# Optimization experiments

Measured on AMD Instinct MI355X. Metric: run time of the kernel, lower is better.

The kernel has to match this reference:

```python
import jax, jax.numpy as jnp
import numpy as np

N = 1_000_000
NUM_CLASSES = 100
N_BINS = 15


def setup_inputs() -> dict:
    key = jax.random.key(0)
    k1, k2 = jax.random.split(key)
    logits = jax.random.normal(k1, (N, NUM_CLASSES), dtype=jnp.float32)
    labels = jax.random.randint(k2, (N,), 0, NUM_CLASSES, dtype=jnp.int64)
    return {"logits": logits, "labels": labels, "n_bins": N_BINS}


def reference(logits, labels, n_bins):
    # softmax -> per-sample confidence (max prob) and prediction (argmax)
    softmaxes = jax.nn.softmax(logits, axis=1)
    confidences = jnp.max(softmaxes, axis=1)
    predictions = jnp.argmax(softmaxes, axis=1).astype(jnp.int32)
    accuracies = (predictions == labels.astype(jnp.int32)).astype(confidences.dtype)

    num_classes = logits.shape[1]
    num_data = logits.shape[0]

    # Bin assignment matching (lower, upper] intervals of linspace(0,1,n_bins+1):
    # conf in ((b)/n_bins, (b+1)/n_bins] -> bin b. conf > 0 always (softmax max).
    bin_idx = jnp.clip(
        jnp.ceil(confidences * n_bins).astype(jnp.int32) - 1, 0, n_bins - 1
    )
    # Fused cell id over (predicted class, bin)
    cell = predictions * n_bins + bin_idx  # [N]
    num_cells = num_classes * n_bins

    sum_conf = jax.ops.segment_sum(confidences, cell, num_segments=num_cells)
    sum_acc = jax.ops.segment_sum(accuracies, cell, num_segments=num_cells)

    # Per non-empty cell: |mean_conf - mean_acc| * count/N = |sum_conf - sum_acc|/N;
    # empty cells contribute exactly 0.
    ece = jnp.sum(jnp.abs(sum_conf - sum_acc)) / num_data
    return ece
```

## Files before the change

### kernel.cpp

```cpp
#include <hip/hip_runtime.h>
#include <math.h>


constexpr int C  = 100;
constexpr int NB = 15;
constexpr int NCELLS = C * NB;

__global__ void ece_zero(float* __restrict__ ws, int n) {
    int i = blockIdx.x * blockDim.x + threadIdx.x;
    if (i < n) ws[i] = 0.0f;
}

__global__ __launch_bounds__(256)
void ece_main(const float* __restrict__ logits,
              const int* __restrict__ labels,
              int N, float* __restrict__ cellsums) {
    __shared__ float hist[2 * NCELLS];
    for (int i = threadIdx.x; i < 2 * NCELLS; i += blockDim.x) hist[i] = 0.0f;
    __syncthreads();

    const int lane4   = threadIdx.x & 3;
    const int group   = (blockIdx.x * blockDim.x + threadIdx.x) >> 2;
    const int ngroups = (gridDim.x * blockDim.x) >> 2;

    for (int row = group; row < N; row += ngroups) {
        const float4* p = reinterpret_cast<const float4*>(logits + (size_t)row * C);

        float4 v[6];
        #pragma unroll
        for (int j = 0; j < 6; ++j) v[j] = p[lane4 + 4 * j];
        const bool has7 = (lane4 == 0);
        float4 v6;
        if (has7) v6 = p[24];

        float m = -INFINITY;
        int   am = 0;
        #pragma unroll
        for (int j = 0; j < 6; ++j) {
            int base = (lane4 + 4 * j) * 4;
            if (v[j].x > m) { m = v[j].x; am = base + 0; }
            if (v[j].y > m) { m = v[j].y; am = base + 1; }
            if (v[j].z > m) { m = v[j].z; am = base + 2; }
            if (v[j].w > m) { m = v[j].w; am = base + 3; }
        }
        if (has7) {
            if (v6.x > m) { m = v6.x; am = 96; }
            if (v6.y > m) { m = v6.y; am = 97; }
            if (v6.z > m) { m = v6.z; am = 98; }
            if (v6.w > m) { m = v6.w; am = 99; }
        }

        #pragma unroll
        for (int off = 1; off < 4; off <<= 1) {
            float om  = __shfl_xor(m, off, 64);
            int   oam = __shfl_xor(am, off, 64);
            if (om > m || (om == m && oam < am)) { m = om; am = oam; }
        }

        float s = 0.0f;
        #pragma unroll
        for (int j = 0; j < 6; ++j) {
            s += __expf(v[j].x - m) + __expf(v[j].y - m)
               + __expf(v[j].z - m) + __expf(v[j].w - m);
        }
        if (has7) {
            s += __expf(v6.x - m) + __expf(v6.y - m)
               + __expf(v6.z - m) + __expf(v6.w - m);
        }
        #pragma unroll
        for (int off = 1; off < 4; off <<= 1) s += __shfl_xor(s, off, 64);

        if (lane4 == 0) {
            float conf = 1.0f / s;
            int b = (int)ceilf(conf * (float)NB) - 1;
            b = b < 0 ? 0 : (b > NB - 1 ? NB - 1 : b);
            int cell = am * NB + b;
            atomicAdd(&hist[cell], conf);
            if (labels[row] == am) atomicAdd(&hist[NCELLS + cell], 1.0f);
        }
    }

    __syncthreads();
    for (int i = threadIdx.x; i < 2 * NCELLS; i += blockDim.x) {
        float v = hist[i];
        if (v != 0.0f) atomicAdd(&cellsums[i], v);
    }
}

__global__ void ece_final(const float* __restrict__ cellsums,
                          float invN, float* __restrict__ out) {
    __shared__ float red[256];
    float t = 0.0f;
    for (int i = threadIdx.x; i < NCELLS; i += blockDim.x)
        t += fabsf(cellsums[i] - cellsums[NCELLS + i]);
    red[threadIdx.x] = t;
    __syncthreads();
    for (int w = 128; w > 0; w >>= 1) {
        if (threadIdx.x < w) red[threadIdx.x] += red[threadIdx.x + w];
        __syncthreads();
    }
    if (threadIdx.x == 0) out[0] = red[0] * invN;
}

extern "C" void kernel_launch(void* const* d_in, const int* in_sizes, int n_in,
                              void* d_out, int out_size, void* d_ws, size_t ws_size,
                              hipStream_t stream) {
    const float* logits = (const float*)d_in[0];
    const int*   labels = (const int*)d_in[1];

    const int N = in_sizes[1];

    float* cellsums = (float*)d_ws;
    float* out = (float*)d_out;

    {
        int n = 2 * NCELLS;
        ece_zero<<<(n + 255) / 256, 256, 0, stream>>>(cellsums, n);
    }

    ece_main<<<2048, 256, 0, stream>>>(logits, labels, N, cellsums);

    ece_final<<<1, 256, 0, stream>>>(cellsums, 1.0f / (float)N, out);
}
```

Measured before the change: 103.6 us.

## Stage logits tiles into LDS via global_load_lds before per-row softmax

The main kernel now copies tiles of 64 rows into padded LDS with the direct global-to-LDS load builtin, using fully contiguous 16-byte lane accesses. Each 4-lane group then reads its row from LDS instead of issuing strided global loads. The grid shrinks to 977 blocks, and exp is rewritten as exp2f of an FMA with log2(e). The aim is better-coalesced, higher-throughput HBM reads. In exchange, each tile costs two block barriers with no double buffering, and the added LDS use per block lowers occupancy.

```diff
diff --git a/kernel.cpp b/kernel.cpp
--- a/kernel.cpp
+++ b/kernel.cpp
@@ -5,82 +5,122 @@
 constexpr int C  = 100;
 constexpr int NB = 15;
 constexpr int NCELLS = C * NB;
+constexpr int ROWS_PER_TILE = 64;
+constexpr int F4_PER_ROW   = 25;
+constexpr int LDS_F4_STRIDE = 26;
+constexpr int LDS_TILE_F4  = ROWS_PER_TILE * LDS_F4_STRIDE;
+constexpr int GRID_MAIN = 977;
 
 __global__ void ece_zero(float* __restrict__ ws, int n) {
     int i = blockIdx.x * blockDim.x + threadIdx.x;
     if (i < n) ws[i] = 0.0f;
 }
 
+__device__ __forceinline__ void load_lds_16B(const void* gsrc, void* ldst) {
+    __builtin_amdgcn_global_load_lds(
+        (const __attribute__((address_space(1))) void*)gsrc,
+        (__attribute__((address_space(3))) void*)ldst, 16, 0, 0);
+}
+
 __global__ __launch_bounds__(256)
 void ece_main(const float* __restrict__ logits,
               const int* __restrict__ labels,
-              int N, float* __restrict__ cellsums) {
-    __shared__ float hist[2 * NCELLS];
+              int N, int ntiles, float* __restrict__ cellsums) {
+    __shared__ float4 stage[LDS_TILE_F4];
+    __shared__ float  hist[2 * NCELLS];
+
     for (int i = threadIdx.x; i < 2 * NCELLS; i += blockDim.x) hist[i] = 0.0f;
-    __syncthreads();
 
-    const int lane4   = threadIdx.x & 3;
-    const int group   = (blockIdx.x * blockDim.x + threadIdx.x) >> 2;
-    const int ngroups = (gridDim.x * blockDim.x) >> 2;
+    const int tid  = threadIdx.x;
+    const int l4   = tid & 3;
+    const int qg   = tid >> 2;
+    const int wbase = (tid >> 6) << 6;
+    const float4* logits4 = reinterpret_cast<const float4*>(logits);
+    constexpr float LOG2E = 1.4426950408889634f;
 
-    for (int row = group; row < N; row += ngroups) {
-        const float4* p = reinterpret_cast<const float4*>(logits + (size_t)row * C);
-
-        float4 v[6];
-        #pragma unroll
-        for (int j = 0; j < 6; ++j) v[j] = p[lane4 + 4 * j];
-        const bool has7 = (lane4 == 0);
-        float4 v6;
-        if (has7) v6 = p[24];
-
-        float m = -INFINITY;
-        int   am = 0;
-        #pragma unroll
-        for (int j = 0; j < 6; ++j) {
-            int base = (lane4 + 4 * j) * 4;
-            if (v[j].x > m) { m = v[j].x; am = base + 0; }
-            if (v[j].y > m) { m = v[j].y; am = base + 1; }
-            if (v[j].z > m) { m = v[j].z; am = base + 2; }
-            if (v[j].w > m) { m = v[j].w; am = base + 3; }
-        }
-        if (has7) {
-            if (v6.x > m) { m = v6.x; am = 96; }
-            if (v6.y > m) { m = v6.y; am = 97; }
-            if (v6.z > m) { m = v6.z; am = 98; }
-            if (v6.w > m) { m = v6.w; am = 99; }
-        }
+    for (int tile = blockIdx.x; tile < ntiles; tile += gridDim.x) {
+        const int row0 = tile * ROWS_PER_TILE;
 
         #pragma unroll
-        for (int off = 1; off < 4; off <<= 1) {
-            float om  = __shfl_xor(m, off, 64);
-            int   oam = __shfl_xor(am, off, 64);
-            if (om > m || (om == m && oam < am)) { m = om; am = oam; }
+        for (int i = 0; i < 7; ++i) {
+            int s = i * 256 + tid;
+            if (s < LDS_TILE_F4) {
+                int r = s / LDS_F4_STRIDE;
+                int c = s - r * LDS_F4_STRIDE;
+                if (c < F4_PER_ROW && (row0 + r) < N) {
+                    const float4* g = logits4 + (size_t)(row0 + r) * F4_PER_ROW + c;
+                    load_lds_16B(g, &stage[i * 256 + wbase]);
+                }
+            }
         }
+        __syncthreads();
 
-        float s = 0.0f;
-        #pragma unroll
-        for (int j = 0; j < 6; ++j) {
-            s += __expf(v[j].x - m) + __expf(v[j].y - m)
-               + __expf(v[j].z - m) + __expf(v[j].w - m);
+        const int row = row0 + qg;
+        if (row < N) {
+            int lab = -1;
+            if (l4 == 0) lab = labels[row];
+
+            const float4* rp = &stage[qg * LDS_F4_STRIDE];
+            float4 v[6];
+            #pragma unroll
+            for (int j = 0; j < 6; ++j) v[j] = rp[l4 + 4 * j];
+            float4 v6;
+            const bool has7 = (l4 == 0);
+            if (has7) v6 = rp[24];
+
+            float m = -INFINITY;
+            int   am = 0;
+            #pragma unroll
+            for (int j = 0; j < 6; ++j) {
+                int base = (l4 + 4 * j) * 4;
+                if (v[j].x > m) { m = v[j].x; am = base + 0; }
+                if (v[j].y > m) { m = v[j].y; am = base + 1; }
+                if (v[j].z > m) { m = v[j].z; am = base + 2; }
+                if (v[j].w > m) { m = v[j].w; am = base + 3; }
+            }
+            if (has7) {
+                if (v6.x > m) { m = v6.x; am = 96; }
+                if (v6.y > m) { m = v6.y; am = 97; }
+                if (v6.z > m) { m = v6.z; am = 98; }
+                if (v6.w > m) { m = v6.w; am = 99; }
+            }
+            #pragma unroll
+            for (int off = 1; off < 4; off <<= 1) {
+                float om  = __shfl_xor(m, off, 64);
+                int   oam = __shfl_xor(am, off, 64);
+                if (om > m || (om == m && oam < am)) { m = om; am = oam; }
+            }
+
+            const float ml = m * LOG2E;
+            float s = 0.0f;
+            #pragma unroll
+            for (int j = 0; j < 6; ++j) {
+                s += exp2f(__fmaf_rn(v[j].x, LOG2E, -ml))
+                   + exp2f(__fmaf_rn(v[j].y, LOG2E, -ml))
+                   + exp2f(__fmaf_rn(v[j].z, LOG2E, -ml))
+                   + exp2f(__fmaf_rn(v[j].w, LOG2E, -ml));
+            }
+            if (has7) {
+                s += exp2f(__fmaf_rn(v6.x, LOG2E, -ml))
+                   + exp2f(__fmaf_rn(v6.y, LOG2E, -ml))
+                   + exp2f(__fmaf_rn(v6.z, LOG2E, -ml))
+                   + exp2f(__fmaf_rn(v6.w, LOG2E, -ml));
+            }
+            #pragma unroll
+            for (int off = 1; off < 4; off <<= 1) s += __shfl_xor(s, off, 64);
+
+            if (l4 == 0) {
+                float conf = 1.0f / s;
+                int b = (int)ceilf(conf * (float)NB) - 1;
+                b = b < 0 ? 0 : (b > NB - 1 ? NB - 1 : b);
+                int cell = am * NB + b;
+                atomicAdd(&hist[cell], conf);
+                if (lab == am) atomicAdd(&hist[NCELLS + cell], 1.0f);
+            }
         }
-        if (has7) {
-            s += __expf(v6.x - m) + __expf(v6.y - m)
-               + __expf(v6.z - m) + __expf(v6.w - m);
-        }
-        #pragma unroll
-        for (int off = 1; off < 4; off <<= 1) s += __shfl_xor(s, off, 64);
-
-        if (lane4 == 0) {
-            float conf = 1.0f / s;
-            int b = (int)ceilf(conf * (float)NB) - 1;
-            b = b < 0 ? 0 : (b > NB - 1 ? NB - 1 : b);
-            int cell = am * NB + b;
-            atomicAdd(&hist[cell], conf);
-            if (labels[row] == am) atomicAdd(&hist[NCELLS + cell], 1.0f);
-        }
+        __syncthreads();
     }
 
-    __syncthreads();
     for (int i = threadIdx.x; i < 2 * NCELLS; i += blockDim.x) {
         float v = hist[i];
         if (v != 0.0f) atomicAdd(&cellsums[i], v);
@@ -109,6 +149,7 @@
     const int*   labels = (const int*)d_in[1];
 
     const int N = in_sizes[1];
+    const int ntiles = (N + ROWS_PER_TILE - 1) / ROWS_PER_TILE;
 
     float* cellsums = (float*)d_ws;
     float* out = (float*)d_out;
@@ -118,7 +159,7 @@
         ece_zero<<<(n + 255) / 256, 256, 0, stream>>>(cellsums, n);
     }
 
-    ece_main<<<2048, 256, 0, stream>>>(logits, labels, N, cellsums);
+    ece_main<<<GRID_MAIN, 256, 0, stream>>>(logits, labels, N, ntiles, cellsums);
 
     ece_final<<<1, 256, 0, stream>>>(cellsums, 1.0f / (float)N, out);
 }
```

Measured after the change: 93.56 us. 9.7% less time.

## Double-buffer logits tiles into LDS via direct global-to-LDS loads

Applied to the files above, without the earlier changes.

Replaces the per-thread register loads of logits with a 64-row tile pipeline. Each tile and its labels are staged in LDS using global_load_lds 16-byte loads, and the next tile is prefetched while the current one is processed, with explicit waitcnt and barriers. Each row is now handled by 16 lanes instead of 4. The exponentials use exp2 with an FMA pre-scale, and the kernel runs as 512 blocks of 1024 threads. It drops the tail handling for N not divisible by 64 and adds two block barriers per tile.

```diff
diff --git a/kernel.cpp b/kernel.cpp
--- a/kernel.cpp
+++ b/kernel.cpp
@@ -5,83 +5,142 @@
 constexpr int C  = 100;
 constexpr int NB = 15;
 constexpr int NCELLS = C * NB;
+constexpr int ROWS = 64;
+constexpr int CHR  = 27;
+constexpr int TILE_CH = ROWS * CHR;
+constexpr int LAB_CH0 = TILE_CH;
+constexpr int BUF_CH  = 2048;
+constexpr int THREADS = 1024;
+constexpr int GRID_MAIN = 512;
 
 __global__ void ece_zero(float* __restrict__ ws, int n) {
     int i = blockIdx.x * blockDim.x + threadIdx.x;
     if (i < n) ws[i] = 0.0f;
 }
 
-__global__ __launch_bounds__(256)
+__device__ __forceinline__ void load_lds_16B(const void* gsrc, void* ldst) {
+    __builtin_amdgcn_global_load_lds(
+        (const __attribute__((address_space(1))) void*)gsrc,
+        (__attribute__((address_space(3))) void*)ldst, 16, 0, 0);
+}
+
+__global__ __launch_bounds__(THREADS, 8)
 void ece_main(const float* __restrict__ logits,
               const int* __restrict__ labels,
-              int N, float* __restrict__ cellsums) {
-    __shared__ float hist[2 * NCELLS];
-    for (int i = threadIdx.x; i < 2 * NCELLS; i += blockDim.x) hist[i] = 0.0f;
+              int ntiles, float* __restrict__ cellsums) {
+    __shared__ float4 stage[2][BUF_CH];
+    __shared__ float  hist[2 * NCELLS];
+
+    for (int i = threadIdx.x; i < 2 * NCELLS; i += THREADS) hist[i] = 0.0f;
     __syncthreads();
 
-    const int lane4   = threadIdx.x & 3;
-    const int group   = (blockIdx.x * blockDim.x + threadIdx.x) >> 2;
-    const int ngroups = (gridDim.x * blockDim.x) >> 2;
+    const int tid = threadIdx.x;
+    const int h   = tid >> 4;
+    const int l   = tid & 15;
 
-    for (int row = group; row < N; row += ngroups) {
-        const float4* p = reinterpret_cast<const float4*>(logits + (size_t)row * C);
+    int r0 = tid / CHR, c0 = tid - r0 * CHR;
+    if (c0 > 24) c0 = 24;
+    const int off0 = (r0 * 25 + c0) * 16;
+    const int s1 = 1024 + tid;
+    int off1; bool isLab = false;
+    if (s1 < TILE_CH) {
+        int r = s1 / CHR, c = s1 - r * CHR;
+        if (c > 24) c = 24;
+        off1 = (r * 25 + c) * 16;
+    } else if (s1 < LAB_CH0 + 16) {
+        isLab = true;
+        off1 = (s1 - LAB_CH0) * 16;
+    } else {
+        off1 = 0;
+    }
+    const size_t dstoff = (size_t)(tid & ~63) * 16;
 
-        float4 v[6];
+    const char* const lg = (const char*)logits;
+    const char* const lb = (const char*)labels;
+    constexpr float LOG2E = 1.4426950408889634f;
+
+#define ISSUE_STAGE(T, BUF)                                                   \
+    {                                                                         \
+        const char* tb_ = lg + (size_t)(T) * (ROWS * C * 4);                  \
+        const char* lt_ = lb + (size_t)(T) * (ROWS * 4);                      \
+        char* d_ = (char*)&stage[(BUF)][0] + dstoff;                          \
+        load_lds_16B(tb_ + off0, d_);                                         \
+        const char* s1p_ = isLab ? (lt_ + off1) : (tb_ + off1);               \
+        load_lds_16B(s1p_, d_ + 1024 * 16);                                   \
+    }
+
+    int t = blockIdx.x;
+    int cur = 0;
+    if (t < ntiles) ISSUE_STAGE(t, 0);
+
+    for (; t < ntiles; t += GRID_MAIN) {
+        const int tn = t + GRID_MAIN;
+        if (tn < ntiles) {
+            ISSUE_STAGE(tn, cur ^ 1);
+            asm volatile("s_waitcnt vmcnt(2)" ::: "memory");
+        } else {
+            asm volatile("s_waitcnt vmcnt(0)" ::: "memory");
+        }
+        __builtin_amdgcn_s_barrier();
+        asm volatile("" ::: "memory");
+
+        const float4* rp = &stage[cur][h * CHR];
+        float4 a = rp[l];
+        float4 b4;
+        const bool two = (l < 9);
+        if (two) b4 = rp[16 + l];
+        const int lab = ((const int*)&stage[cur][LAB_CH0])[h];
+
+        float m = a.x; int am = 4 * l;
+        if (a.y > m) { m = a.y; am = 4 * l + 1; }
+        if (a.z > m) { m = a.z; am = 4 * l + 2; }
+        if (a.w > m) { m = a.w; am = 4 * l + 3; }
+        if (two) {
+            const int e = 64 + 4 * l;
+            if (b4.x > m) { m = b4.x; am = e; }
+            if (b4.y > m) { m = b4.y; am = e + 1; }
+            if (b4.z > m) { m = b4.z; am = e + 2; }
+            if (b4.w > m) { m = b4.w; am = e + 3; }
+        }
         #pragma unroll
-        for (int j = 0; j < 6; ++j) v[j] = p[lane4 + 4 * j];
-        const bool has7 = (lane4 == 0);
-        float4 v6;
-        if (has7) v6 = p[24];
-
-        float m = -INFINITY;
-        int   am = 0;
-        #pragma unroll
-        for (int j = 0; j < 6; ++j) {
-            int base = (lane4 + 4 * j) * 4;
-            if (v[j].x > m) { m = v[j].x; am = base + 0; }
-            if (v[j].y > m) { m = v[j].y; am = base + 1; }
-            if (v[j].z > m) { m = v[j].z; am = base + 2; }
-            if (v[j].w > m) { m = v[j].w; am = base + 3; }
-        }
-        if (has7) {
-            if (v6.x > m) { m = v6.x; am = 96; }
-            if (v6.y > m) { m = v6.y; am = 97; }
-            if (v6.z > m) { m = v6.z; am = 98; }
-            if (v6.w > m) { m = v6.w; am = 99; }
-        }
-
-        #pragma unroll
-        for (int off = 1; off < 4; off <<= 1) {
+        for (int off = 1; off < 16; off <<= 1) {
             float om  = __shfl_xor(m, off, 64);
             int   oam = __shfl_xor(am, off, 64);
             if (om > m || (om == m && oam < am)) { m = om; am = oam; }
         }
 
-        float s = 0.0f;
-        #pragma unroll
-        for (int j = 0; j < 6; ++j) {
-            s += __expf(v[j].x - m) + __expf(v[j].y - m)
-               + __expf(v[j].z - m) + __expf(v[j].w - m);
-        }
-        if (has7) {
-            s += __expf(v6.x - m) + __expf(v6.y - m)
-               + __expf(v6.z - m) + __expf(v6.w - m);
+        const float ml = m * LOG2E;
+        float s = exp2f(__fmaf_rn(a.x, LOG2E, -ml))
+                + exp2f(__fmaf_rn(a.y, LOG2E, -ml))
+                + exp2f(__fmaf_rn(a.z, LOG2E, -ml))
+                + exp2f(__fmaf_rn(a.w, LOG2E, -ml));
+        if (two) {
+            s += exp2f(__fmaf_rn(b4.x, LOG2E, -ml))
+               + exp2f(__fmaf_rn(b4.y, LOG2E, -ml))
+               + exp2f(__fmaf_rn(b4.z, LOG2E, -ml))
+               + exp2f(__fmaf_rn(b4.w, LOG2E, -ml));
         }
         #pragma unroll
-        for (int off = 1; off < 4; off <<= 1) s += __shfl_xor(s, off, 64);
+        for (int off = 1; off < 16; off <<= 1) s += __shfl_xor(s, off, 64);
 
-        if (lane4 == 0) {
+        if (l == 0) {
             float conf = 1.0f / s;
             int b = (int)ceilf(conf * (float)NB) - 1;
             b = b < 0 ? 0 : (b > NB - 1 ? NB - 1 : b);
             int cell = am * NB + b;
             atomicAdd(&hist[cell], conf);
-            if (labels[row] == am) atomicAdd(&hist[NCELLS + cell], 1.0f);
+            if (lab == am) atomicAdd(&hist[NCELLS + cell], 1.0f);
         }
+
+        asm volatile("s_waitcnt lgkmcnt(0)" ::: "memory");
+        __builtin_amdgcn_s_barrier();
+        asm volatile("" ::: "memory");
+        cur ^= 1;
     }
+#undef ISSUE_STAGE
 
     __syncthreads();
-    for (int i = threadIdx.x; i < 2 * NCELLS; i += blockDim.x) {
+    for (int i = threadIdx.x; i < 2 * NCELLS; i += THREADS) {
         float v = hist[i];
         if (v != 0.0f) atomicAdd(&cellsums[i], v);
     }
@@ -109,6 +168,7 @@
     const int*   labels = (const int*)d_in[1];
 
     const int N = in_sizes[1];
+    const int ntiles = N / ROWS;
 
     float* cellsums = (float*)d_ws;
     float* out = (float*)d_out;
@@ -118,7 +178,7 @@
         ece_zero<<<(n + 255) / 256, 256, 0, stream>>>(cellsums, n);
     }
 
-    ece_main<<<2048, 256, 0, stream>>>(logits, labels, N, cellsums);
+    ece_main<<<GRID_MAIN, THREADS, 0, stream>>>(logits, labels, ntiles, cellsums);
 
     ece_final<<<1, 256, 0, stream>>>(cellsums, 1.0f / (float)N, out);
 }
```

After: 108.4 us. 4.6% more time.
